# Kernel optimization log

Hardware: AMD Instinct MI355X
Metric: run time of the kernel (lower is better)

Reference implementation:

```python
import jax, jax.numpy as jnp
import numpy as np

B, K, V, D = 8, 4, 32000, 1024          # batch, beam, vocab, d_model
PAD, BOS, EOS = 0, 1, 2
MAX_SEQ_LEN = 32                        # bos + generated tokens
ALPHA = 0.6                             # length penalty (len_pen)
NEG_INF = -1e9


def setup_inputs() -> dict:
    key = jax.random.key(0)
    k1, k2, k3 = jax.random.split(key, 3)
    return {
        "emb_table": jax.random.normal(k1, (V, D), jnp.float32) * 0.02,
        "W_dec": jax.random.normal(k2, (D, D), jnp.float32) * 0.02,
        "b_dec": jnp.zeros((D,), jnp.float32),
        "W_out": jax.random.normal(k3, (D, V), jnp.float32) * 0.02,
    }


def _beam_search(emb_table, W_dec, b_dec, W_out):
    def step_log_probs(tokens):  # tokens: int [N] -> log_probs [N, V]
        h = jnp.tanh(emb_table[tokens] @ W_dec + b_dec)
        return jax.nn.log_softmax(h @ W_out, axis=-1)

    # ---- initial step from <bos>: topk over vocab gives the K initial beams
    lp0 = step_log_probs(jnp.full((B,), BOS, jnp.int32))      # [B, V]
    scores, first_tok = jax.lax.top_k(lp0, K)                 # [B, K]

    seqs = jnp.full((B, K, MAX_SEQ_LEN), PAD, jnp.int32)
    seqs = seqs.at[:, :, 0].set(BOS).at[:, :, 1].set(first_tok)
    finished = first_tok == EOS                               # [B, K] bool
    lengths = jnp.ones((B, K), jnp.float32)                   # generated tokens

    # finished beams may only continue with <pad> at zero added log-prob
    pad_row = jnp.full((V,), NEG_INF, jnp.float32).at[PAD].set(0.0)

    def body(carry, t):
        seqs, scores, finished, lengths, last_tok = carry
        lp = step_log_probs(last_tok.reshape(B * K)).reshape(B, K, V)
        lp = jnp.where(finished[..., None], pad_row, lp)
        cand = (scores[..., None] + lp).reshape(B, K * V)     # [B, K*V]
        scores, idx = jax.lax.top_k(cand, K)                  # [B, K]
        beam = idx // V                                       # source beam
        tok = (idx % V).astype(jnp.int32)                     # next token
        # beam reorder (gather) of all per-beam state
        seqs = jnp.take_along_axis(seqs, beam[..., None], axis=1)
        finished = jnp.take_along_axis(finished, beam, axis=1)
        lengths = jnp.take_along_axis(lengths, beam, axis=1)
        lengths = lengths + (~finished).astype(lengths.dtype)
        finished = finished | (tok == EOS)
        seqs = seqs.at[:, :, t].set(tok)
        return (seqs, scores, finished, lengths, tok), None

    carry = (seqs, scores, finished, lengths, first_tok)
    (seqs, scores, finished, lengths, _), _ = jax.lax.scan(
        body, carry, jnp.arange(2, MAX_SEQ_LEN)
    )
    # https://arxiv.org/pdf/1609.08144.pdf length penalty
    len_pen = ((5.0 + lengths) / 6.0) ** ALPHA
    return seqs, scores / len_pen


def reference(emb_table, W_dec, b_dec, W_out):
    return _beam_search(emb_table, W_dec, b_dec, W_out)
```

## Files before the change

### kernel.cpp

```cpp
#include <hip/hip_runtime.h>
#include <math.h>
#include <limits.h>

#define BATCH 8
#define BEAM 4
#define VOCAB 32000
#define DMODEL 1024
#define MAXSEQ 32
#define PAD_ID 0
#define BOS_ID 1
#define EOS_ID 2
#define NROWS 32
#define NBLK 500
#define NPART 512

#define HT_OFF     0
#define PMS_OFF    131072
#define PV_OFF     262144
#define PI_OFF     524288
#define STATE_OFF  786432

__device__ __forceinline__ bool better(float av, int ai, float bv, int bi) {
  return (av > bv) || ((av == bv) && (ai < bi));
}

template<int N>
__device__ __forceinline__ void insN(float v, int i, float tv[N], int ti[N]) {
  if (better(v, i, tv[N-1], ti[N-1])) {
    tv[N-1] = v; ti[N-1] = i;
    #pragma unroll
    for (int j = N-1; j > 0; j--) {
      if (better(tv[j], ti[j], tv[j-1], ti[j-1])) {
        float fv = tv[j]; tv[j] = tv[j-1]; tv[j-1] = fv;
        int ii = ti[j]; ti[j] = ti[j-1]; ti[j-1] = ii;
      }
    }
  }
}

__device__ __forceinline__ void row_partials(
    float v, int c, int row, int p, int lane,
    float2* __restrict__ PMS, float4* __restrict__ PV, int4* __restrict__ PI) {
  float m = v;
  #pragma unroll
  for (int off = 32; off >= 1; off >>= 1) m = fmaxf(m, __shfl_xor(m, off));
  float s = expf(v - m);
  #pragma unroll
  for (int off = 32; off >= 1; off >>= 1) s += __shfl_xor(s, off);
  float myv = v; int myc = c; bool alive = true;
  float t4v[4]; int t4i[4];
  #pragma unroll
  for (int q = 0; q < 4; ++q) {
    float cv = alive ? myv : -INFINITY;
    int   ci = alive ? myc : INT_MAX;
    #pragma unroll
    for (int off = 32; off >= 1; off >>= 1) {
      float ov = __shfl_xor(cv, off);
      int   oi = __shfl_xor(ci, off);
      if (better(ov, oi, cv, ci)) { cv = ov; ci = oi; }
    }
    t4v[q] = cv; t4i[q] = ci;
    alive = alive && (ci != myc);
  }
  if (lane == 0) {
    PMS[row * NPART + p] = make_float2(m, s);
    PV[row * NPART + p]  = make_float4(t4v[0], t4v[1], t4v[2], t4v[3]);
    PI[row * NPART + p]  = make_int4(t4i[0], t4i[1], t4i[2], t4i[3]);
  }
}

template<bool INIT>
__global__ __launch_bounds__(256) void k_embdec(
    const float* __restrict__ emb, const float* __restrict__ Wdec,
    const float* __restrict__ bdec, const int* __restrict__ last_tok,
    float* __restrict__ hT) {
  __shared__ float red[4][2][64];
  int tid = threadIdx.x;
  int lane = tid & 63, wv = tid >> 6;
  int c = blockIdx.x * 64 + lane;
  int r0 = blockIdx.y * 2;
  int t0 = INIT ? BOS_ID : last_tok[r0];
  int t1 = INIT ? BOS_ID : last_tok[r0 + 1];
  const float* x0 = emb + (size_t)t0 * DMODEL + wv * 256;
  const float* x1 = emb + (size_t)t1 * DMODEL + wv * 256;
  const float* W  = Wdec + (size_t)(wv * 256) * DMODEL + c;
  float a0 = 0.f, a1 = 0.f;
  #pragma unroll 16
  for (int j = 0; j < 256; ++j) {
    float w = W[(size_t)j * DMODEL];
    a0 = fmaf(x0[j], w, a0);
    a1 = fmaf(x1[j], w, a1);
  }
  red[wv][0][lane] = a0;
  red[wv][1][lane] = a1;
  __syncthreads();
  if (wv == 0) {
    a0 = (red[0][0][lane] + red[1][0][lane]) + (red[2][0][lane] + red[3][0][lane]);
    a1 = (red[0][1][lane] + red[1][1][lane]) + (red[2][1][lane] + red[3][1][lane]);
    float bb = bdec[c];
    hT[(size_t)c * NROWS + r0]     = tanhf(a0 + bb);
    hT[(size_t)c * NROWS + r0 + 1] = tanhf(a1 + bb);
  }
}

template<int NR>
__global__ __launch_bounds__(512, 4) void k_logits_v3(
    const float* __restrict__ hT, const float* __restrict__ Wout,
    float2* __restrict__ PMS, float4* __restrict__ PV, int4* __restrict__ PI) {
  constexpr int NCH = NR / 8;
  constexpr int NG  = NR / 4;
  __shared__ __attribute__((aligned(16))) float sH[8192];
  __shared__ __attribute__((aligned(16))) float red[4096];

  int tid = threadIdx.x;
  int lane = tid & 63;
  int kw  = tid >> 6;
  int c = blockIdx.x * 64 + lane;
  int p = blockIdx.x;

  float acc[NR];
  #pragma unroll
  for (int r = 0; r < NR; ++r) acc[r] = 0.f;

  const float* wcol = Wout + c;

  #pragma unroll 1
  for (int pass = 0; pass < 4; ++pass) {
    const float4* src = (const float4*)(hT + pass * 8192) + (size_t)tid * 4;
    float4 v0 = src[0], v1 = src[1], v2 = src[2], v3 = src[3];
    __syncthreads();
    {
      float4* dst = (float4*)sH + (size_t)tid * 4;
      dst[0] = v0; dst[1] = v1; dst[2] = v2; dst[3] = v3;
    }
    __syncthreads();

    const float* wp = wcol + (size_t)(pass * 256 + kw * 32) * VOCAB;
    const float* hb0 = sH + (kw * 32) * 32;
    #pragma unroll
    for (int u = 0; u < 32; ++u) {
      float w = wp[(size_t)u * VOCAB];
      #pragma unroll
      for (int g = 0; g < NG; ++g) {
        float4 h4 = *(const float4*)(hb0 + u * 32 + g * 4);
        acc[g * 4 + 0] = fmaf(h4.x, w, acc[g * 4 + 0]);
        acc[g * 4 + 1] = fmaf(h4.y, w, acc[g * 4 + 1]);
        acc[g * 4 + 2] = fmaf(h4.z, w, acc[g * 4 + 2]);
        acc[g * 4 + 3] = fmaf(h4.w, w, acc[g * 4 + 3]);
      }
    }
  }

  __syncthreads();
  #pragma unroll 1
  for (int cc = 0; cc < NCH; ++cc) {
    #pragma unroll
    for (int r8 = 0; r8 < 8; ++r8)
      red[(kw * 8 + r8) * 64 + lane] = acc[cc * 8 + r8];
    __syncthreads();
    float v = ((((((red[(0 * 8 + kw) * 64 + lane]
                  + red[(1 * 8 + kw) * 64 + lane])
                  + red[(2 * 8 + kw) * 64 + lane])
                  + red[(3 * 8 + kw) * 64 + lane])
                  + red[(4 * 8 + kw) * 64 + lane])
                  + red[(5 * 8 + kw) * 64 + lane])
                  + red[(6 * 8 + kw) * 64 + lane])
                  + red[(7 * 8 + kw) * 64 + lane];
    row_partials(v, c, cc * 8 + kw, p, lane, PMS, PV, PI);
    __syncthreads();
  }
}

template<bool INIT>
__global__ __launch_bounds__(256) void k_batch(
    const float2* __restrict__ PMS, const float4* __restrict__ PV,
    const int4* __restrict__ PI,
    int* __restrict__ seqs, float* __restrict__ scores,
    int* __restrict__ finished, float* __restrict__ lengths,
    int* __restrict__ last_tok, int t, int wout, float* __restrict__ out) {
  __shared__ float s_lse[BEAM], s_base[BEAM];
  __shared__ int   s_fin[BEAM];
  __shared__ float s_v4[BEAM][4];
  __shared__ int   s_i4[BEAM][4];
  __shared__ float s_score[4];
  __shared__ int   s_beam[4], s_tok[4];

  int b = blockIdx.x, tid = threadIdx.x;
  int lane = tid & 63, wv = tid >> 6;
  const int R = INIT ? 1 : BEAM;

  if (wv < R) {
    int row = INIT ? b : b * BEAM + wv;
    float M = -INFINITY, S = 0.f;
    float lv[4]; int li[4];
    #pragma unroll
    for (int j = 0; j < 4; ++j) { lv[j] = -INFINITY; li[j] = INT_MAX; }
    for (int p = lane; p < NBLK; p += 64) {
      float2 ms = PMS[row * NPART + p];
      float4 pv = PV[row * NPART + p];
      int4   pi = PI[row * NPART + p];
      if (ms.x > M) { S = S * expf(M - ms.x) + ms.y; M = ms.x; }
      else          { S += ms.y * expf(ms.x - M); }
      insN<4>(pv.x, pi.x, lv, li);
      insN<4>(pv.y, pi.y, lv, li);
      insN<4>(pv.z, pi.z, lv, li);
      insN<4>(pv.w, pi.w, lv, li);
    }
    #pragma unroll
    for (int off = 32; off >= 1; off >>= 1) {
      float oM = __shfl_xor(M, off);
      float oS = __shfl_xor(S, off);
      float nM = fmaxf(M, oM);
      S = S * expf(M - nM) + oS * expf(oM - nM);
      M = nM;
    }
    int ptr = 0;
    float o4v[4]; int o4i[4];
    #pragma unroll
    for (int q = 0; q < 4; ++q) {
      float hv = -INFINITY; int hi = INT_MAX;
      #pragma unroll
      for (int j = 0; j < 4; ++j) { if (ptr == j) { hv = lv[j]; hi = li[j]; } }
      float cv = hv; int ci = hi;
      #pragma unroll
      for (int off = 32; off >= 1; off >>= 1) {
        float ov = __shfl_xor(cv, off);
        int   oi = __shfl_xor(ci, off);
        if (better(ov, oi, cv, ci)) { cv = ov; ci = oi; }
      }
      o4v[q] = cv; o4i[q] = ci;
      if (ci == hi && ci != INT_MAX) ptr++;
    }
    if (lane == 0) {
      s_lse[wv] = M + logf(S);
      #pragma unroll
      for (int q = 0; q < 4; ++q) { s_v4[wv][q] = o4v[q]; s_i4[wv][q] = o4i[q]; }
      s_base[wv] = INIT ? 0.f : scores[row];
      s_fin[wv]  = INIT ? 0 : finished[row];
    }
  }
  __syncthreads();

  if (tid == 0) {
    float fv[4]; int fi[4];
    #pragma unroll
    for (int q = 0; q < 4; ++q) { fv[q] = -INFINITY; fi[q] = INT_MAX; }
    for (int kk = 0; kk < R; ++kk) {
      if (s_fin[kk]) {
        insN<4>(s_base[kk], kk * VOCAB + PAD_ID, fv, fi);
      } else {
        float base = s_base[kk], lse = s_lse[kk];
        #pragma unroll
        for (int j = 0; j < 4; ++j)
          insN<4>(base + (s_v4[kk][j] - lse), kk * VOCAB + s_i4[kk][j], fv, fi);
      }
    }
    #pragma unroll
    for (int q = 0; q < 4; ++q) {
      s_score[q] = fv[q];
      s_beam[q]  = fi[q] / VOCAB;
      s_tok[q]   = fi[q] % VOCAB;
    }
  }
  __syncthreads();

  int k5 = tid >> 5, p5 = tid & 31;
  if (INIT) {
    if (tid < 128) {
      int val = (p5 == 0) ? BOS_ID : ((p5 == 1) ? s_tok[k5] : PAD_ID);
      seqs[(b * BEAM + k5) * MAXSEQ + p5] = val;
    }
    if (tid < 4) {
      scores[b * BEAM + tid]   = s_score[tid];
      finished[b * BEAM + tid] = (s_tok[tid] == EOS_ID) ? 1 : 0;
      lengths[b * BEAM + tid]  = 1.f;
      last_tok[b * BEAM + tid] = s_tok[tid];
    }
  } else {
    int sv = 0, oldfin = 0; float oldlen = 0.f;
    if (tid < 128) {
      sv = seqs[(b * BEAM + s_beam[k5]) * MAXSEQ + p5];
      if (p5 == t) sv = s_tok[k5];
    }
    if (tid < 4) {
      oldfin = finished[b * BEAM + s_beam[tid]];
      oldlen = lengths[b * BEAM + s_beam[tid]];
    }
    __syncthreads();
    if (tid < 128) {
      seqs[(b * BEAM + k5) * MAXSEQ + p5] = sv;
      if (wout) out[(b * BEAM + k5) * MAXSEQ + p5] = (float)sv;
    }
    if (tid < 4) {
      float nl = oldlen + (oldfin ? 0.f : 1.f);
      int   nf = (oldfin || (s_tok[tid] == EOS_ID)) ? 1 : 0;
      scores[b * BEAM + tid]   = s_score[tid];
      finished[b * BEAM + tid] = nf;
      lengths[b * BEAM + tid]  = nl;
      last_tok[b * BEAM + tid] = s_tok[tid];
      if (wout)
        out[BATCH * BEAM * MAXSEQ + b * BEAM + tid] =
            s_score[tid] / powf((5.f + nl) / 6.f, 0.6f);
    }
  }
}

extern "C" void kernel_launch(void* const* d_in, const int* in_sizes, int n_in,
                              void* d_out, int out_size, void* d_ws, size_t ws_size,
                              hipStream_t stream) {
  const float* emb  = (const float*)d_in[0];
  const float* Wdec = (const float*)d_in[1];
  const float* bdec = (const float*)d_in[2];
  const float* Wout = (const float*)d_in[3];
  float* out = (float*)d_out;

  char* ws = (char*)d_ws;
  float*  hT  = (float*) (ws + HT_OFF);
  float2* PMS = (float2*)(ws + PMS_OFF);
  float4* PV  = (float4*)(ws + PV_OFF);
  int4*   PI  = (int4*)  (ws + PI_OFF);
  int*   seqs     = (int*)  (ws + STATE_OFF);
  float* scores   = (float*)(ws + STATE_OFF + 4096);
  int*   finished = (int*)  (ws + STATE_OFF + 4224);
  float* lengths  = (float*)(ws + STATE_OFF + 4352);
  int*   last_tok = (int*)  (ws + STATE_OFF + 4480);

  k_embdec<true><<<dim3(DMODEL / 64, BATCH / 2), 256, 0, stream>>>(
      emb, Wdec, bdec, last_tok, hT);
  k_logits_v3<8><<<NBLK, 512, 0, stream>>>(hT, Wout, PMS, PV, PI);
  k_batch<true><<<BATCH, 256, 0, stream>>>(PMS, PV, PI, seqs, scores, finished,
                                           lengths, last_tok, 0, 0, out);

  for (int t = 2; t < MAXSEQ; t++) {
    k_embdec<false><<<dim3(DMODEL / 64, NROWS / 2), 256, 0, stream>>>(
        emb, Wdec, bdec, last_tok, hT);
    k_logits_v3<32><<<NBLK, 512, 0, stream>>>(hT, Wout, PMS, PV, PI);
    k_batch<false><<<BATCH, 256, 0, stream>>>(PMS, PV, PI, seqs, scores,
                                              finished, lengths, last_tok, t,
                                              (t == MAXSEQ - 1) ? 1 : 0, out);
  }
}
```

Baseline: 2.366 ms.

## Compute two vocab column groups per block in logits kernel to reuse hidden tile

Adds a new logits kernel in which each block covers 128 vocab columns (two 64-column partitions) instead of 64, so each hidden-state tile staged in shared memory feeds twice as many FMAs. The grid is halved to 250 blocks and each thread keeps two 32-row accumulator sets. This cuts shared-memory traffic and repeated hT loads per unit of work. The cost is doubled accumulator register pressure, which may lower occupancy, and fewer blocks than the GPU has compute units.

```diff
diff --git a/kernel.cpp b/kernel.cpp
--- a/kernel.cpp
+++ b/kernel.cpp
@@ -12,6 +12,7 @@
 #define EOS_ID 2
 #define NROWS 32
 #define NBLK 500
+#define NBLK2 250
 #define NPART 512
 
 #define HT_OFF     0
@@ -66,6 +67,28 @@
     PMS[row * NPART + p] = make_float2(m, s);
     PV[row * NPART + p]  = make_float4(t4v[0], t4v[1], t4v[2], t4v[3]);
     PI[row * NPART + p]  = make_int4(t4i[0], t4i[1], t4i[2], t4i[3]);
+  }
+}
+
+__device__ __forceinline__ void reduce_and_emit(
+    const float (&acc)[NROWS], float* red, int c, int p, int kw, int lane,
+    float2* __restrict__ PMS, float4* __restrict__ PV, int4* __restrict__ PI) {
+  #pragma unroll 1
+  for (int cc = 0; cc < 4; ++cc) {
+    #pragma unroll
+    for (int r8 = 0; r8 < 8; ++r8)
+      red[(kw * 8 + r8) * 64 + lane] = acc[cc * 8 + r8];
+    __syncthreads();
+    float v = ((((((red[(0 * 8 + kw) * 64 + lane]
+                  + red[(1 * 8 + kw) * 64 + lane])
+                  + red[(2 * 8 + kw) * 64 + lane])
+                  + red[(3 * 8 + kw) * 64 + lane])
+                  + red[(4 * 8 + kw) * 64 + lane])
+                  + red[(5 * 8 + kw) * 64 + lane])
+                  + red[(6 * 8 + kw) * 64 + lane])
+                  + red[(7 * 8 + kw) * 64 + lane];
+    row_partials(v, c, cc * 8 + kw, p, lane, PMS, PV, PI);
+    __syncthreads();
   }
 }
 
@@ -171,6 +194,61 @@
   }
 }
 
+__global__ __launch_bounds__(512, 4) void k_logits_v4(
+    const float* __restrict__ hT, const float* __restrict__ Wout,
+    float2* __restrict__ PMS, float4* __restrict__ PV, int4* __restrict__ PI) {
+  __shared__ __attribute__((aligned(16))) float sH[8192];
+  __shared__ __attribute__((aligned(16))) float red[4096];
+
+  int tid = threadIdx.x;
+  int lane = tid & 63;
+  int kw  = tid >> 6;
+  int cA = blockIdx.x * 128 + lane;
+  int p0 = blockIdx.x * 2;
+
+  float accA[NROWS], accB[NROWS];
+  #pragma unroll
+  for (int r = 0; r < NROWS; ++r) { accA[r] = 0.f; accB[r] = 0.f; }
+
+  const float* wcol = Wout + cA;
+
+  #pragma unroll 1
+  for (int pass = 0; pass < 4; ++pass) {
+    const float4* src = (const float4*)(hT + pass * 8192) + (size_t)tid * 4;
+    float4 v0 = src[0], v1 = src[1], v2 = src[2], v3 = src[3];
+    __syncthreads();
+    {
+      float4* dst = (float4*)sH + (size_t)tid * 4;
+      dst[0] = v0; dst[1] = v1; dst[2] = v2; dst[3] = v3;
+    }
+    __syncthreads();
+
+    const float* wp = wcol + (size_t)(pass * 256 + kw * 32) * VOCAB;
+    const float* hb0 = sH + (kw * 32) * 32;
+    #pragma unroll 8
+    for (int u = 0; u < 32; ++u) {
+      float wA = wp[(size_t)u * VOCAB];
+      float wB = wp[(size_t)u * VOCAB + 64];
+      #pragma unroll
+      for (int g = 0; g < 8; ++g) {
+        float4 h4 = *(const float4*)(hb0 + u * 32 + g * 4);
+        accA[g * 4 + 0] = fmaf(h4.x, wA, accA[g * 4 + 0]);
+        accA[g * 4 + 1] = fmaf(h4.y, wA, accA[g * 4 + 1]);
+        accA[g * 4 + 2] = fmaf(h4.z, wA, accA[g * 4 + 2]);
+        accA[g * 4 + 3] = fmaf(h4.w, wA, accA[g * 4 + 3]);
+        accB[g * 4 + 0] = fmaf(h4.x, wB, accB[g * 4 + 0]);
+        accB[g * 4 + 1] = fmaf(h4.y, wB, accB[g * 4 + 1]);
+        accB[g * 4 + 2] = fmaf(h4.z, wB, accB[g * 4 + 2]);
+        accB[g * 4 + 3] = fmaf(h4.w, wB, accB[g * 4 + 3]);
+      }
+    }
+  }
+
+  __syncthreads();
+  reduce_and_emit(accA, red, cA,      p0,     kw, lane, PMS, PV, PI);
+  reduce_and_emit(accB, red, cA + 64, p0 + 1, kw, lane, PMS, PV, PI);
+}
+
 template<bool INIT>
 __global__ __launch_bounds__(256) void k_batch(
     const float2* __restrict__ PMS, const float4* __restrict__ PV,
@@ -334,7 +412,7 @@
   for (int t = 2; t < MAXSEQ; t++) {
     k_embdec<false><<<dim3(DMODEL / 64, NROWS / 2), 256, 0, stream>>>(
         emb, Wdec, bdec, last_tok, hT);
-    k_logits_v3<32><<<NBLK, 512, 0, stream>>>(hT, Wout, PMS, PV, PI);
+    k_logits_v4<<<NBLK2, 512, 0, stream>>>(hT, Wout, PMS, PV, PI);
     k_batch<false><<<BATCH, 256, 0, stream>>>(PMS, PV, PI, seqs, scores,
                                               finished, lengths, last_tok, t,
                                               (t == MAXSEQ - 1) ? 1 : 0, out);
```

Result: slower. 3.007 ms (+27.1%).

## Add 1024-thread logits kernel splitting D across 16 waves per column tile

Applied to the files above, without the earlier changes.

Introduces a new logits kernel in which each 1024-thread block covers 64 vocab columns and splits the 1024-long reduction across 16 waves of 64 rows each. hT is read directly from global memory rather than staged in shared memory, and partial sums are combined through a 32 KB shared buffer in four chunks before the per-row partial top-k and log-sum-exp. It also fully unrolls the chunk reduction loop in the old kernel. The aim is more memory-level parallelism and latency hiding when streaming W_out, at the cost of larger blocks, extra reduction traffic and per-block synchronisation.

```diff
diff --git a/kernel.cpp b/kernel.cpp
--- a/kernel.cpp
+++ b/kernel.cpp
@@ -152,7 +152,7 @@
   }
 
   __syncthreads();
-  #pragma unroll 1
+  #pragma unroll
   for (int cc = 0; cc < NCH; ++cc) {
     #pragma unroll
     for (int r8 = 0; r8 < 8; ++r8)
@@ -168,6 +168,55 @@
                   + red[(7 * 8 + kw) * 64 + lane];
     row_partials(v, c, cc * 8 + kw, p, lane, PMS, PV, PI);
     __syncthreads();
+  }
+}
+
+__global__ __launch_bounds__(1024) void k_logits_v7(
+    const float* __restrict__ hT, const float* __restrict__ Wout,
+    float2* __restrict__ PMS, float4* __restrict__ PV, int4* __restrict__ PI) {
+  __shared__ __attribute__((aligned(16))) float red[8192];
+
+  int tid = threadIdx.x;
+  int lane = tid & 63;
+  int kw  = tid >> 6;
+  int c = blockIdx.x * 64 + lane;
+  int p = blockIdx.x;
+
+  float acc[NROWS];
+  #pragma unroll
+  for (int r = 0; r < NROWS; ++r) acc[r] = 0.f;
+
+  const float* wp = Wout + (size_t)(kw * 64) * VOCAB + c;
+  const float* hb = hT + (kw * 64) * NROWS;
+
+  #pragma unroll 4
+  for (int u = 0; u < 64; ++u) {
+    float w = wp[(size_t)u * VOCAB];
+    const float* h = hb + u * NROWS;
+    #pragma unroll
+    for (int g = 0; g < 8; ++g) {
+      float4 h4 = *(const float4*)(h + g * 4);
+      acc[g * 4 + 0] = fmaf(h4.x, w, acc[g * 4 + 0]);
+      acc[g * 4 + 1] = fmaf(h4.y, w, acc[g * 4 + 1]);
+      acc[g * 4 + 2] = fmaf(h4.z, w, acc[g * 4 + 2]);
+      acc[g * 4 + 3] = fmaf(h4.w, w, acc[g * 4 + 3]);
+    }
+  }
+
+  #pragma unroll
+  for (int cc = 0; cc < 4; ++cc) {
+    __syncthreads();
+    #pragma unroll
+    for (int r8 = 0; r8 < 8; ++r8)
+      red[(kw * 8 + r8) * 64 + lane] = acc[cc * 8 + r8];
+    __syncthreads();
+    if (kw < 8) {
+      float v = red[(0 * 8 + kw) * 64 + lane];
+      #pragma unroll
+      for (int s = 1; s < 16; ++s)
+        v += red[(s * 8 + kw) * 64 + lane];
+      row_partials(v, c, cc * 8 + kw, p, lane, PMS, PV, PI);
+    }
   }
 }
 
@@ -334,7 +383,7 @@
   for (int t = 2; t < MAXSEQ; t++) {
     k_embdec<false><<<dim3(DMODEL / 64, NROWS / 2), 256, 0, stream>>>(
         emb, Wdec, bdec, last_tok, hT);
-    k_logits_v3<32><<<NBLK, 512, 0, stream>>>(hT, Wout, PMS, PV, PI);
+    k_logits_v7<<<NBLK, 1024, 0, stream>>>(hT, Wout, PMS, PV, PI);
     k_batch<false><<<BATCH, 256, 0, stream>>>(PMS, PV, PI, seqs, scores,
                                               finished, lengths, last_tok, t,
                                               (t == MAXSEQ - 1) ? 1 : 0, out);
```

New measurement: 5.214 ms. 120% more time.

## Split logits GEMV into 1000 narrower blocks with half-wave row partials

Applied to the files above, without the earlier changes.

Adds a new logits kernel for the 32-row decode steps. It uses 32 vocab columns per block over 1000 blocks, splits each wave into two 32-lane halves that cover different row groups, and does a single cross-wave reduction instead of four chunked ones. The partial buffers grow to 1024 slots per row, and that path is chosen only when the workspace is large enough. The aim is more blocks and more memory-level parallelism on the Wout stream, at the cost of twice as many partials for the batch top-k merge and narrower 128-byte column loads.

```diff
diff --git a/kernel.cpp b/kernel.cpp
--- a/kernel.cpp
+++ b/kernel.cpp
@@ -12,13 +12,8 @@
 #define EOS_ID 2
 #define NROWS 32
 #define NBLK 500
-#define NPART 512
-
-#define HT_OFF     0
-#define PMS_OFF    131072
-#define PV_OFF     262144
-#define PI_OFF     524288
-#define STATE_OFF  786432
+#define NBLK32 1000
+#define HT_OFF 0
 
 __device__ __forceinline__ bool better(float av, int ai, float bv, int bi) {
   return (av > bv) || ((av == bv) && (ai < bi));
@@ -38,8 +33,8 @@
   }
 }
 
-__device__ __forceinline__ void row_partials(
-    float v, int c, int row, int p, int lane,
+__device__ __forceinline__ void row_partials64(
+    float v, int c, int row, int p, int lane, int npart,
     float2* __restrict__ PMS, float4* __restrict__ PV, int4* __restrict__ PI) {
   float m = v;
   #pragma unroll
@@ -63,9 +58,40 @@
     alive = alive && (ci != myc);
   }
   if (lane == 0) {
-    PMS[row * NPART + p] = make_float2(m, s);
-    PV[row * NPART + p]  = make_float4(t4v[0], t4v[1], t4v[2], t4v[3]);
-    PI[row * NPART + p]  = make_int4(t4i[0], t4i[1], t4i[2], t4i[3]);
+    PMS[row * npart + p] = make_float2(m, s);
+    PV[row * npart + p]  = make_float4(t4v[0], t4v[1], t4v[2], t4v[3]);
+    PI[row * npart + p]  = make_int4(t4i[0], t4i[1], t4i[2], t4i[3]);
+  }
+}
+
+__device__ __forceinline__ void row_partials32(
+    float v, int c, int row, int p, int c5, int npart,
+    float2* __restrict__ PMS, float4* __restrict__ PV, int4* __restrict__ PI) {
+  float m = v;
+  #pragma unroll
+  for (int off = 16; off >= 1; off >>= 1) m = fmaxf(m, __shfl_xor(m, off, 32));
+  float s = expf(v - m);
+  #pragma unroll
+  for (int off = 16; off >= 1; off >>= 1) s += __shfl_xor(s, off, 32);
+  float myv = v; int myc = c; bool alive = true;
+  float t4v[4]; int t4i[4];
+  #pragma unroll
+  for (int q = 0; q < 4; ++q) {
+    float cv = alive ? myv : -INFINITY;
+    int   ci = alive ? myc : INT_MAX;
+    #pragma unroll
+    for (int off = 16; off >= 1; off >>= 1) {
+      float ov = __shfl_xor(cv, off, 32);
+      int   oi = __shfl_xor(ci, off, 32);
+      if (better(ov, oi, cv, ci)) { cv = ov; ci = oi; }
+    }
+    t4v[q] = cv; t4i[q] = ci;
+    alive = alive && (ci != myc);
+  }
+  if (c5 == 0) {
+    PMS[row * npart + p] = make_float2(m, s);
+    PV[row * npart + p]  = make_float4(t4v[0], t4v[1], t4v[2], t4v[3]);
+    PI[row * npart + p]  = make_int4(t4i[0], t4i[1], t4i[2], t4i[3]);
   }
 }
 
@@ -106,7 +132,8 @@
 template<int NR>
 __global__ __launch_bounds__(512, 4) void k_logits_v3(
     const float* __restrict__ hT, const float* __restrict__ Wout,
-    float2* __restrict__ PMS, float4* __restrict__ PV, int4* __restrict__ PI) {
+    float2* __restrict__ PMS, float4* __restrict__ PV, int4* __restrict__ PI,
+    int npart) {
   constexpr int NCH = NR / 8;
   constexpr int NG  = NR / 4;
   __shared__ __attribute__((aligned(16))) float sH[8192];
@@ -152,7 +179,7 @@
   }
 
   __syncthreads();
-  #pragma unroll 1
+  #pragma unroll
   for (int cc = 0; cc < NCH; ++cc) {
     #pragma unroll
     for (int r8 = 0; r8 < 8; ++r8)
@@ -166,15 +193,84 @@
                   + red[(5 * 8 + kw) * 64 + lane])
                   + red[(6 * 8 + kw) * 64 + lane])
                   + red[(7 * 8 + kw) * 64 + lane];
-    row_partials(v, c, cc * 8 + kw, p, lane, PMS, PV, PI);
-    __syncthreads();
+    row_partials64(v, c, cc * 8 + kw, p, lane, npart, PMS, PV, PI);
+    __syncthreads();
+  }
+}
+
+__global__ __launch_bounds__(512) void k_logits_v8(
+    const float* __restrict__ hT, const float* __restrict__ Wout,
+    float2* __restrict__ PMS, float4* __restrict__ PV, int4* __restrict__ PI,
+    int npart) {
+  __shared__ __attribute__((aligned(16))) float sH[4096];
+  __shared__ __attribute__((aligned(16))) float red[8192];
+
+  int tid = threadIdx.x;
+  int lane = tid & 63;
+  int kw  = tid >> 6;
+  int h   = lane >> 5;
+  int c5  = lane & 31;
+  int c = blockIdx.x * 32 + c5;
+  int p = blockIdx.x;
+
+  float acc[16];
+  #pragma unroll
+  for (int r = 0; r < 16; ++r) acc[r] = 0.f;
+
+  const float* wcol = Wout + c;
+
+  #pragma unroll 1
+  for (int pass = 0; pass < 8; ++pass) {
+    const float4* src = (const float4*)(hT + pass * 4096) + (size_t)tid * 2;
+    float4 v0 = src[0], v1 = src[1];
+    __syncthreads();
+    {
+      float4* dst = (float4*)sH + (size_t)tid * 2;
+      dst[0] = v0; dst[1] = v1;
+    }
+    __syncthreads();
+
+    const float* wp = wcol + (size_t)(pass * 128 + kw * 16) * VOCAB;
+    const float* hb0 = sH + (kw * 16) * 32 + h * 16;
+    #pragma unroll
+    for (int u = 0; u < 16; ++u) {
+      float w = wp[(size_t)u * VOCAB];
+      #pragma unroll
+      for (int q = 0; q < 4; ++q) {
+        float4 h4 = *(const float4*)(hb0 + u * 32 + q * 4);
+        acc[q * 4 + 0] = fmaf(h4.x, w, acc[q * 4 + 0]);
+        acc[q * 4 + 1] = fmaf(h4.y, w, acc[q * 4 + 1]);
+        acc[q * 4 + 2] = fmaf(h4.z, w, acc[q * 4 + 2]);
+        acc[q * 4 + 3] = fmaf(h4.w, w, acc[q * 4 + 3]);
+      }
+    }
+  }
+
+  __syncthreads();
+  #pragma unroll
+  for (int j = 0; j < 16; ++j)
+    red[(kw * 32 + h * 16 + j) * 32 + c5] = acc[j];
+  __syncthreads();
+
+  #pragma unroll
+  for (int it = 0; it < 2; ++it) {
+    int row = kw + h * 8 + it * 16;
+    float v = ((((((red[(0 * 32 + row) * 32 + c5]
+                  + red[(1 * 32 + row) * 32 + c5])
+                  + red[(2 * 32 + row) * 32 + c5])
+                  + red[(3 * 32 + row) * 32 + c5])
+                  + red[(4 * 32 + row) * 32 + c5])
+                  + red[(5 * 32 + row) * 32 + c5])
+                  + red[(6 * 32 + row) * 32 + c5])
+                  + red[(7 * 32 + row) * 32 + c5];
+    row_partials32(v, c, row, p, c5, npart, PMS, PV, PI);
   }
 }
 
 template<bool INIT>
 __global__ __launch_bounds__(256) void k_batch(
     const float2* __restrict__ PMS, const float4* __restrict__ PV,
-    const int4* __restrict__ PI,
+    const int4* __restrict__ PI, int npart, int nslots,
     int* __restrict__ seqs, float* __restrict__ scores,
     int* __restrict__ finished, float* __restrict__ lengths,
     int* __restrict__ last_tok, int t, int wout, float* __restrict__ out) {
@@ -195,10 +291,10 @@
     float lv[4]; int li[4];
     #pragma unroll
     for (int j = 0; j < 4; ++j) { lv[j] = -INFINITY; li[j] = INT_MAX; }
-    for (int p = lane; p < NBLK; p += 64) {
-      float2 ms = PMS[row * NPART + p];
-      float4 pv = PV[row * NPART + p];
-      int4   pi = PI[row * NPART + p];
+    for (int p = lane; p < nslots; p += 64) {
+      float2 ms = PMS[row * npart + p];
+      float4 pv = PV[row * npart + p];
+      int4   pi = PI[row * npart + p];
       if (ms.x > M) { S = S * expf(M - ms.x) + ms.y; M = ms.x; }
       else          { S += ms.y * expf(ms.x - M); }
       insN<4>(pv.x, pi.x, lv, li);
@@ -315,28 +411,45 @@
   float* out = (float*)d_out;
 
   char* ws = (char*)d_ws;
+  const size_t base = 131072;
+  size_t need1024 = base + (size_t)1024 * NROWS * (8 + 16 + 16) + 4608;
+  int npart = (ws_size >= need1024) ? 1024 : 512;
+
+  size_t pms_off = base;
+  size_t pv_off  = pms_off + (size_t)npart * NROWS * 8;
+  size_t pi_off  = pv_off  + (size_t)npart * NROWS * 16;
+  size_t st_off  = pi_off  + (size_t)npart * NROWS * 16;
+
   float*  hT  = (float*) (ws + HT_OFF);
-  float2* PMS = (float2*)(ws + PMS_OFF);
-  float4* PV  = (float4*)(ws + PV_OFF);
-  int4*   PI  = (int4*)  (ws + PI_OFF);
-  int*   seqs     = (int*)  (ws + STATE_OFF);
-  float* scores   = (float*)(ws + STATE_OFF + 4096);
-  int*   finished = (int*)  (ws + STATE_OFF + 4224);
-  float* lengths  = (float*)(ws + STATE_OFF + 4352);
-  int*   last_tok = (int*)  (ws + STATE_OFF + 4480);
+  float2* PMS = (float2*)(ws + pms_off);
+  float4* PV  = (float4*)(ws + pv_off);
+  int4*   PI  = (int4*)  (ws + pi_off);
+  int*   seqs     = (int*)  (ws + st_off);
+  float* scores   = (float*)(ws + st_off + 4096);
+  int*   finished = (int*)  (ws + st_off + 4224);
+  float* lengths  = (float*)(ws + st_off + 4352);
+  int*   last_tok = (int*)  (ws + st_off + 4480);
 
   k_embdec<true><<<dim3(DMODEL / 64, BATCH / 2), 256, 0, stream>>>(
       emb, Wdec, bdec, last_tok, hT);
-  k_logits_v3<8><<<NBLK, 512, 0, stream>>>(hT, Wout, PMS, PV, PI);
-  k_batch<true><<<BATCH, 256, 0, stream>>>(PMS, PV, PI, seqs, scores, finished,
-                                           lengths, last_tok, 0, 0, out);
+  k_logits_v3<8><<<NBLK, 512, 0, stream>>>(hT, Wout, PMS, PV, PI, npart);
+  k_batch<true><<<BATCH, 256, 0, stream>>>(PMS, PV, PI, npart, NBLK, seqs,
+                                           scores, finished, lengths, last_tok,
+                                           0, 0, out);
 
   for (int t = 2; t < MAXSEQ; t++) {
     k_embdec<false><<<dim3(DMODEL / 64, NROWS / 2), 256, 0, stream>>>(
         emb, Wdec, bdec, last_tok, hT);
-    k_logits_v3<32><<<NBLK, 512, 0, stream>>>(hT, Wout, PMS, PV, PI);
-    k_batch<false><<<BATCH, 256, 0, stream>>>(PMS, PV, PI, seqs, scores,
-                                              finished, lengths, last_tok, t,
-                                              (t == MAXSEQ - 1) ? 1 : 0, out);
-  }
-}
+    if (npart == 1024) {
+      k_logits_v8<<<NBLK32, 512, 0, stream>>>(hT, Wout, PMS, PV, PI, npart);
+      k_batch<false><<<BATCH, 256, 0, stream>>>(
+          PMS, PV, PI, npart, NBLK32, seqs, scores, finished, lengths,
+          last_tok, t, (t == MAXSEQ - 1) ? 1 : 0, out);
+    } else {
+      k_logits_v3<32><<<NBLK, 512, 0, stream>>>(hT, Wout, PMS, PV, PI, npart);
+      k_batch<false><<<BATCH, 256, 0, stream>>>(
+          PMS, PV, PI, npart, NBLK, seqs, scores, finished, lengths,
+          last_tok, t, (t == MAXSEQ - 1) ? 1 : 0, out);
+    }
+  }
+}
```

Result: slower. 2.615 ms (+10.5%).
